# Performance work log

Hardware: AMD Instinct MI355X
Metric: run time of the kernel (lower is better)

The kernel has to match this reference:

```python
import jax, jax.numpy as jnp
import numpy as np

B, C, HH, WW, QK = 8, 64, 64, 64, 8


def setup_inputs() -> dict:
    key = jax.random.key(0)
    ks = jax.random.split(key, 22)
    s = 0.05
    def W(k, o, i):
        return jax.random.normal(k, (o, i), jnp.float32) * s
    def bvec(k, o):
        return jax.random.normal(k, (o,), jnp.float32) * s
    return {
        "H_in": jax.random.normal(ks[0], (B, C, HH, WW), jnp.float32),
        "M_prev": jax.random.normal(ks[1], (B, C, HH, WW), jnp.float32),
        "wq": W(ks[2], QK, C), "bq": bvec(ks[3], QK),
        "wkh": W(ks[4], QK, C), "bkh": bvec(ks[5], QK),
        "wvh": W(ks[6], C, C), "bvh": bvec(ks[7], C),
        "wkm": W(ks[8], QK, C), "bkm": bvec(ks[9], QK),
        "wvm": W(ks[10], C, C), "bvm": bvec(ks[11], C),
        "wz": W(ks[12], C, 2 * C), "bz": bvec(ks[13], C),
        "wo": W(ks[14], C, 2 * C), "bo": bvec(ks[15], C),
        "wg": W(ks[16], C, 2 * C), "bg": bvec(ks[17], C),
        "wi": W(ks[18], C, 2 * C), "bi": bvec(ks[19], C),
    }


def _conv1x1(w, b, x):
    # x: [B, Cin, N] -> [B, Cout, N]
    return jnp.einsum("oc,bcn->bon", w, x) + b[None, :, None]


def reference(H_in, M_prev, wq, bq, wkh, bkh, wvh, bvh, wkm, bkm, wvm, bvm,
              wz, bz, wo, bo, wg, bg, wi, bi):
    Bn, Cn, Hn, Wn = H_in.shape
    N = Hn * Wn
    h = H_in.reshape(Bn, Cn, N)   # flatten spatial
    m = M_prev.reshape(Bn, Cn, N)

    Q = _conv1x1(wq, bq, h)       # [B, QK, N]
    Kh = _conv1x1(wkh, bkh, h)
    Vh = _conv1x1(wvh, bvh, h)    # [B, C, N]
    Km = _conv1x1(wkm, bkm, m)
    Vm = _conv1x1(wvm, bvm, m)

    scale = jnp.asarray(np.sqrt(Q.shape[1]), Q.dtype)
    # scores: [B, N, N], softmax over last axis
    Ah = jax.nn.softmax(jnp.einsum("bcn,bcm->bnm", Q, Kh) / scale, axis=-1)
    Am = jax.nn.softmax(jnp.einsum("bcn,bcm->bnm", Q, Km) / scale, axis=-1)
    # Zh = Vh @ Ah^T : [B, C, N]
    Zh = jnp.einsum("bcm,bnm->bcn", Vh, Ah)
    Zm = jnp.einsum("bcm,bnm->bcn", Vm, Am)

    Z = _conv1x1(wz, bz, jnp.concatenate([Zh, Zm], axis=1))  # [B, C, N]
    concat = jnp.concatenate([h, Z], axis=1)                  # [B, 2C, N]
    O_t = jax.nn.sigmoid(_conv1x1(wo, bo, concat))
    G_t = jnp.tanh(_conv1x1(wg, bg, concat))
    I_t = jax.nn.sigmoid(_conv1x1(wi, bi, concat))

    M_t = (1.0 - I_t) * m + I_t * G_t
    H_out = O_t * M_t
    return (H_out.reshape(Bn, Cn, Hn, Wn), M_t.reshape(Bn, Cn, Hn, Wn))
```

## Files before the change

### kernel.cpp

```cpp
#include <hip/hip_runtime.h>

#define BATCH 8
#define CC 64
#define NN 4096
#define SCL 0.51006973f

typedef __attribute__((ext_vector_type(8))) short s16x8;
typedef __attribute__((ext_vector_type(4))) short s16x4;
typedef __attribute__((ext_vector_type(4))) float f32x4;
typedef __attribute__((ext_vector_type(2))) unsigned int uint2v;

__device__ __forceinline__ short f2bf(float f) {
  unsigned u = __builtin_bit_cast(unsigned, f);
  u += 0x7fffu + ((u >> 16) & 1u);
  return (short)(u >> 16);
}

__device__ __forceinline__ unsigned cvt_pk_bf16(float lo, float hi) {
  unsigned r;
  asm volatile("v_cvt_pk_bf16_f32 %0, %1, %2" : "=v"(r) : "v"(lo), "v"(hi));
  return r;
}

__device__ __forceinline__ int kperm(int kk) {
  int hh = (kk >> 5) & 1, g = (kk >> 3) & 3, c = kk & 7;
  return hh * 32 + (c < 4 ? (g << 2) + c : 16 + ((g ^ 2) << 2) + (c - 4));
}

__global__ void prep_weights_kernel(const float* __restrict__ wz, const float* __restrict__ bz,
                                    const float* __restrict__ wo, const float* __restrict__ bo,
                                    const float* __restrict__ wg, const float* __restrict__ bg,
                                    const float* __restrict__ wi, const float* __restrict__ bi,
                                    const float* __restrict__ wq, const float* __restrict__ bq,
                                    const float* __restrict__ wkh, const float* __restrict__ bkh,
                                    const float* __restrict__ wvh, const float* __restrict__ bvh,
                                    const float* __restrict__ wkm, const float* __restrict__ bkm,
                                    const float* __restrict__ wvm, const float* __restrict__ bvm,
                                    short* __restrict__ Weff, float* __restrict__ beff,
                                    short* __restrict__ Wcat, float* __restrict__ bias) {
  int i = blockIdx.x * 256 + threadIdx.x;
  const float* wjs[3] = {wo, wg, wi};
  const float* bjs[3] = {bo, bg, bi};
  const float gsc[3] = {1.44269504f, 2.88539008f, 1.44269504f};
  if (i < 36864) {
    int j = i / 12288, rem = i % 12288, o = rem / 192, k = rem % 192;
    const float* wj = wjs[j];
    float v;
    if (k < 64) {
      v = wj[o * 128 + k];
    } else {
      v = 0.f;
      #pragma unroll 8
      for (int t = 0; t < 64; ++t) v += wj[o * 128 + 64 + t] * wz[t * 128 + (k - 64)];
    }
    Weff[i] = f2bf(v * gsc[j]);
  } else if (i < 37056) {
    int i2 = i - 36864;
    int j = i2 >> 6, o = i2 & 63;
    const float* wj = wjs[j];
    float v = bjs[j][o];
    #pragma unroll 8
    for (int t = 0; t < 64; ++t) v += wj[o * 128 + 64 + t] * bz[t];
    beff[i2] = v * gsc[j];
  } else if (i < 47296) {
    int i2 = i - 37056;
    int src = i2 / 5120, rem = i2 % 5120, row = rem >> 6, col = rem & 63;
    float v;
    if (src == 0) {
      if (row < 64) v = wvh[row * 64 + col];
      else if (row < 72) v = wq[(row - 64) * 64 + col] * SCL;
      else v = wkh[(row - 72) * 64 + col];
    } else {
      if (row < 64) v = wvm[row * 64 + col];
      else if (row < 72) v = wkm[(row - 64) * 64 + col];
      else v = 0.f;
    }
    Wcat[i2] = f2bf(v);
  } else if (i < 47456) {
    int i3 = i - 47296;
    int src = i3 / 80, row = i3 % 80;
    float v;
    if (src == 0) v = (row < 64) ? bvh[row] : (row < 72 ? bq[row - 64] * SCL : bkh[row - 72]);
    else          v = (row < 64) ? bvm[row] : (row < 72 ? bkm[row - 64] : 0.f);
    bias[i3] = v;
  }
}

__global__ __launch_bounds__(256) void proj_kernel(
    const float* __restrict__ H_in, const float* __restrict__ M_prev,
    const short* __restrict__ Wcat, const float* __restrict__ bias,
    short* __restrict__ Qt, short* __restrict__ Kht, short* __restrict__ Kmt,
    short* __restrict__ Vh, short* __restrict__ Vm) {
  int src = blockIdx.x & 1;
  int n0 = ((blockIdx.x >> 1) & 31) << 7;
  int b = blockIdx.x >> 6;
  int tid = threadIdx.x, w = tid >> 6, l = tid & 63, lg = l >> 4, ll = l & 15;

  const float* __restrict__ X = src ? M_prev : H_in;
  short* __restrict__ Vp = src ? Vm : Vh;

  __shared__ __align__(16) short Xt[128][68];

  {
    int nl = tid & 127, chalf = (tid >> 7) << 5;
    int n = n0 + nl;
    #pragma unroll
    for (int cg = 0; cg < 8; ++cg) {
      int c = chalf + cg * 4;
      float v0 = X[((size_t)((b << 6) + c + 0)) * NN + n];
      float v1 = X[((size_t)((b << 6) + c + 1)) * NN + n];
      float v2 = X[((size_t)((b << 6) + c + 2)) * NN + n];
      float v3 = X[((size_t)((b << 6) + c + 3)) * NN + n];
      uint2v pk;
      pk.x = cvt_pk_bf16(v0, v1);
      pk.y = cvt_pk_bf16(v2, v3);
      *(uint2v*)&Xt[nl][c] = pk;
    }
  }
  __syncthreads();

  f32x4 acc[5][2];
  #pragma unroll
  for (int ot = 0; ot < 5; ++ot)
    #pragma unroll
    for (int ns = 0; ns < 2; ++ns)
      #pragma unroll
      for (int r = 0; r < 4; ++r) acc[ot][ns][r] = bias[src * 80 + ot * 16 + lg * 4 + r];

  #pragma unroll
  for (int kk = 0; kk < 2; ++kk) {
    s16x8 aw[5];
    #pragma unroll
    for (int ot = 0; ot < 5; ++ot)
      aw[ot] = *(const s16x8*)(Wcat + ((size_t)(src * 80 + ot * 16 + ll)) * 64 + kk * 32 + lg * 8);
    #pragma unroll
    for (int ns = 0; ns < 2; ++ns) {
      s16x8 bx = *(const s16x8*)&Xt[w * 32 + ns * 16 + ll][kk * 32 + lg * 8];
      #pragma unroll
      for (int ot = 0; ot < 5; ++ot)
        acc[ot][ns] = __builtin_amdgcn_mfma_f32_16x16x32_bf16(aw[ot], bx, acc[ot][ns], 0, 0, 0);
    }
  }

  #pragma unroll
  for (int ns = 0; ns < 2; ++ns) {
    int n = n0 + w * 32 + ns * 16 + ll;
    #pragma unroll
    for (int ot = 0; ot < 4; ++ot) {
      #pragma unroll
      for (int r = 0; r < 4; ++r) {
        int o = ot * 16 + lg * 4 + r;
        Vp[((size_t)((b << 6) + o)) * NN + n] = f2bf(acc[ot][ns][r]);
      }
    }
    int pr = (n & ~63) + kperm(n & 63);
    #pragma unroll
    for (int r = 0; r < 4; ++r) {
      float v = acc[4][ns][r];
      if (src == 0) {
        if (lg < 2) Qt[((size_t)(b * NN + n)) * 8 + (lg * 4 + r)] = f2bf(v);
        else        Kht[((size_t)(b * NN + pr)) * 8 + ((lg - 2) * 4 + r)] = f2bf(v);
      } else {
        if (lg < 2) Kmt[((size_t)(b * NN + pr)) * 8 + (lg * 4 + r)] = f2bf(v);
      }
    }
  }
}

__global__ __launch_bounds__(256) void attn_kernel(
    const short* __restrict__ Qt, const short* __restrict__ Kht, const short* __restrict__ Kmt,
    const short* __restrict__ Vh, const short* __restrict__ Vm, short* __restrict__ Zt) {
  unsigned vb = (blockIdx.x & 7) * 128 + (blockIdx.x >> 3);
  int b  = vb >> 7;
  int s  = (vb >> 6) & 1;
  int q0 = (vb & 63) << 6;
  int tid = threadIdx.x;
  int w = tid >> 6, l = tid & 63, lg = l >> 4, ll = l & 15;

  const short* __restrict__ Kp = s ? Kmt : Kht;
  const short* __restrict__ Vp = s ? Vm : Vh;

  __shared__ __align__(16) short Vt[2][64][128];
  __shared__ __align__(16) short Ktl[2][128][8];

  s16x8 bq = {};
  if (lg == 0) bq = *(const s16x8*)(Qt + ((size_t)(b * NN + q0 + w * 16 + ll)) * 8);
  s16x8 ones;
  #pragma unroll
  for (int i = 0; i < 8; ++i) ones[i] = (short)0x3F80;

  f32x4 accZ[4];
  f32x4 accDn = {0.f, 0.f, 0.f, 0.f};
  #pragma unroll
  for (int cs = 0; cs < 4; ++cs) accZ[cs] = (f32x4){0.f, 0.f, 0.f, 0.f};

  const bool lo32 = (l < 32);

  #define STAGE(buf_, k0_)                                                                   \
    do {                                                                                     \
      _Pragma("unroll")                                                                      \
      for (int j = 0; j < 4; ++j) {                                                          \
        int brow = j * 16 + w * 4;                                                           \
        int row = brow + (l >> 4);                                                           \
        int slot = l & 15;                                                                   \
        const short* src = Vp + ((size_t)((b << 6) + row)) * NN + (k0_) +                    \
                           ((slot ^ (row & 7)) << 3);                                        \
        __builtin_amdgcn_global_load_lds((const __attribute__((address_space(1))) void*)src, \
            (__attribute__((address_space(3))) void*)&Vt[buf_][brow][0], 16, 0, 0);          \
      }                                                                                      \
      if (w == 0) {                                                                          \
        _Pragma("unroll")                                                                    \
        for (int jk = 0; jk < 2; ++jk) {                                                     \
          const short* srck = Kp + ((size_t)(b * NN) + (k0_) + jk * 64 + l) * 8;             \
          __builtin_amdgcn_global_load_lds((const __attribute__((address_space(1))) void*)srck,\
              (__attribute__((address_space(3))) void*)&Ktl[buf_][jk * 64][0], 16, 0, 0);    \
        }                                                                                    \
      }                                                                                      \
    } while (0)

  STAGE(0, 0);
  int buf = 0;
  for (int kt = 0; kt < 32; ++kt) {
    asm volatile("s_waitcnt vmcnt(0)" ::: "memory");
    __builtin_amdgcn_s_barrier();
    if (kt < 31) { STAGE(buf ^ 1, (kt + 1) << 7); }

    #pragma unroll
    for (int s2 = 0; s2 < 2; ++s2) {
      float p[4][4];
      #pragma unroll
      for (int hh = 0; hh < 2; ++hh) {
        #pragma unroll
        for (int par = 0; par < 2; ++par) {
          s16x8 ak = *(const s16x8*)&Ktl[buf][s2 * 64 + hh * 32 + par * 16 + ll][0];
          f32x4 sc = __builtin_amdgcn_mfma_f32_16x16x32_bf16(ak, bq, (f32x4){0.f,0.f,0.f,0.f}, 0, 0, 0);
          #pragma unroll
          for (int r = 0; r < 4; ++r) p[hh * 2 + par][r] = __builtin_amdgcn_exp2f(sc[r]);
        }
      }
      unsigned wkv[4][2];
      #pragma unroll
      for (int ks = 0; ks < 4; ++ks) {
        wkv[ks][0] = cvt_pk_bf16(p[ks][0], p[ks][1]);
        wkv[ks][1] = cvt_pk_bf16(p[ks][2], p[ks][3]);
      }
      #pragma unroll
      for (int hh = 0; hh < 2; ++hh) {
        unsigned o0 = wkv[hh * 2 + 1][0], o1 = wkv[hh * 2 + 1][1];
        uint2v pr0 = __builtin_amdgcn_permlane32_swap(o0, o0, false, false);
        uint2v pr1 = __builtin_amdgcn_permlane32_swap(o1, o1, false, false);
        unsigned sw0 = lo32 ? pr0.y : pr0.x;
        unsigned sw1 = lo32 ? pr1.y : pr1.x;
        union { unsigned u[4]; s16x8 v; } bpu;
        bpu.u[0] = wkv[hh * 2][0];
        bpu.u[1] = wkv[hh * 2][1];
        bpu.u[2] = sw0;
        bpu.u[3] = sw1;
        s16x8 bp = bpu.v;
        accDn = __builtin_amdgcn_mfma_f32_16x16x32_bf16(ones, bp, accDn, 0, 0, 0);
        #pragma unroll
        for (int cs = 0; cs < 4; ++cs) {
          int row = cs * 16 + ll;
          int slot = (s2 << 3) + ((hh * 4 + lg) ^ (row & 7));
          s16x8 av = *(const s16x8*)((const short*)&Vt[buf][0][0] + row * 128 + slot * 8);
          accZ[cs] = __builtin_amdgcn_mfma_f32_16x16x32_bf16(av, bp, accZ[cs], 0, 0, 0);
        }
      }
    }
    buf ^= 1;
  }

  float rd = __builtin_amdgcn_rcpf(accDn[0]);
  #pragma unroll
  for (int cs = 0; cs < 4; ++cs) {
    s16x4 o4;
    #pragma unroll
    for (int r = 0; r < 4; ++r) o4[r] = f2bf(accZ[cs][r] * rd);
    *(s16x4*)(Zt + ((size_t)(b * NN + q0 + w * 16 + ll)) * 128 + s * 64 + cs * 16 + lg * 4) = o4;
  }
  #undef STAGE
}

__global__ __launch_bounds__(256) void gates_kernel(
    const float* __restrict__ H_in, const float* __restrict__ M_prev,
    const short* __restrict__ Zt, const short* __restrict__ Weff,
    const float* __restrict__ beff, float* __restrict__ out) {
  int b = blockIdx.x >> 6;
  int n0 = (blockIdx.x & 63) << 6;
  int tid = threadIdx.x, w = tid >> 6, l = tid & 63, lg = l >> 4, ll = l & 15;
  __shared__ __align__(16) short Xt[64][200];

  for (int i = tid; i < 512; i += 256) {
    int k = i >> 3, ns = i & 7;
    const float* src = H_in + ((size_t)((b << 6) + k)) * NN + n0 + ns * 8;
    #pragma unroll
    for (int j2 = 0; j2 < 8; ++j2) Xt[ns * 8 + j2][k] = f2bf(src[j2]);
  }
  for (int i = tid; i < 1024; i += 256) {
    int n = i >> 4, seg = i & 15;
    *(s16x8*)&Xt[n][64 + seg * 8] =
        *(const s16x8*)(Zt + ((size_t)(b * NN + n0 + n)) * 128 + seg * 8);
  }
  __syncthreads();

  f32x4 acc[3][4];
  #pragma unroll
  for (int j = 0; j < 3; ++j) {
    float bj = beff[j * 64 + w * 16 + lg * 4];
    float bj1 = beff[j * 64 + w * 16 + lg * 4 + 1];
    float bj2 = beff[j * 64 + w * 16 + lg * 4 + 2];
    float bj3 = beff[j * 64 + w * 16 + lg * 4 + 3];
    #pragma unroll
    for (int ns = 0; ns < 4; ++ns) {
      acc[j][ns][0] = bj; acc[j][ns][1] = bj1; acc[j][ns][2] = bj2; acc[j][ns][3] = bj3;
    }
  }

  #pragma unroll
  for (int kk = 0; kk < 6; ++kk) {
    s16x8 aw[3];
    #pragma unroll
    for (int j = 0; j < 3; ++j)
      aw[j] = *(const s16x8*)(Weff + ((size_t)(j * 64 + w * 16 + ll)) * 192 + kk * 32 + lg * 8);
    #pragma unroll
    for (int ns = 0; ns < 4; ++ns) {
      s16x8 bx = *(const s16x8*)&Xt[ns * 16 + ll][kk * 32 + lg * 8];
      #pragma unroll
      for (int j = 0; j < 3; ++j)
        acc[j][ns] = __builtin_amdgcn_mfma_f32_16x16x32_bf16(aw[j], bx, acc[j][ns], 0, 0, 0);
    }
  }

  float* Hout = out;
  float* Mout = out + (size_t)BATCH * CC * NN;
  #pragma unroll
  for (int ns = 0; ns < 4; ++ns) {
    #pragma unroll
    for (int r = 0; r < 4; ++r) {
      int c = w * 16 + lg * 4 + r;
      int n = n0 + ns * 16 + ll;
      size_t idx = ((size_t)((b << 6) + c)) * NN + n;
      float xo = acc[0][ns][r], xg = acc[1][ns][r], xi = acc[2][ns][r];
      float o  = __builtin_amdgcn_rcpf(1.f + __builtin_amdgcn_exp2f(-xo));
      float g  = 2.f * __builtin_amdgcn_rcpf(1.f + __builtin_amdgcn_exp2f(-xg)) - 1.f;
      float ii = __builtin_amdgcn_rcpf(1.f + __builtin_amdgcn_exp2f(-xi));
      float m  = M_prev[idx];
      float mt = (1.f - ii) * m + ii * g;
      Mout[idx] = mt;
      Hout[idx] = o * mt;
    }
  }
}

extern "C" void kernel_launch(void* const* d_in, const int* in_sizes, int n_in,
                              void* d_out, int out_size, void* d_ws, size_t ws_size,
                              hipStream_t stream) {
  (void)in_sizes; (void)n_in; (void)out_size; (void)ws_size;
  const float* H_in  = (const float*)d_in[0];
  const float* M_prev= (const float*)d_in[1];
  const float* wq  = (const float*)d_in[2];
  const float* bq  = (const float*)d_in[3];
  const float* wkh = (const float*)d_in[4];
  const float* bkh = (const float*)d_in[5];
  const float* wvh = (const float*)d_in[6];
  const float* bvh = (const float*)d_in[7];
  const float* wkm = (const float*)d_in[8];
  const float* bkm = (const float*)d_in[9];
  const float* wvm = (const float*)d_in[10];
  const float* bvm = (const float*)d_in[11];
  const float* wz  = (const float*)d_in[12];
  const float* bz  = (const float*)d_in[13];
  const float* wo  = (const float*)d_in[14];
  const float* bo  = (const float*)d_in[15];
  const float* wg  = (const float*)d_in[16];
  const float* bg  = (const float*)d_in[17];
  const float* wi  = (const float*)d_in[18];
  const float* bi  = (const float*)d_in[19];

  char* ws = (char*)d_ws;
  size_t off = 0;
  auto alloc = [&](size_t bytes) -> void* {
    void* p = ws + off;
    off += (bytes + 255) & ~(size_t)255;
    return p;
  };
  short* Weff = (short*)alloc(3 * 64 * 192 * 2);
  float* beff = (float*)alloc(192 * 4);
  short* Wcat = (short*)alloc(2 * 80 * 64 * 2);
  float* bias = (float*)alloc(160 * 4);
  short* Qt   = (short*)alloc((size_t)BATCH * NN * 8 * 2);
  short* Kht  = (short*)alloc((size_t)BATCH * NN * 8 * 2);
  short* Kmt  = (short*)alloc((size_t)BATCH * NN * 8 * 2);
  short* Vh   = (short*)alloc((size_t)BATCH * CC * NN * 2);
  short* Vm   = (short*)alloc((size_t)BATCH * CC * NN * 2);
  short* Zt   = (short*)alloc((size_t)BATCH * NN * 128 * 2);

  prep_weights_kernel<<<186, 256, 0, stream>>>(wz, bz, wo, bo, wg, bg, wi, bi,
                                               wq, bq, wkh, bkh, wvh, bvh, wkm, bkm, wvm, bvm,
                                               Weff, beff, Wcat, bias);
  proj_kernel<<<512, 256, 0, stream>>>(H_in, M_prev, Wcat, bias, Qt, Kht, Kmt, Vh, Vm);
  attn_kernel<<<1024, 256, 0, stream>>>(Qt, Kht, Kmt, Vh, Vm, Zt);
  gates_kernel<<<512, 256, 0, stream>>>(H_in, M_prev, Zt, Weff, beff, (float*)d_out);
}
```

Before: 190.3 us.

## Split attention key range across two blocks and combine partials in gates kernel

The attention kernel now splits the 4096 keys into two halves handled by separate blocks, doubling the grid to 2048 blocks. Each block writes unnormalized partial Z and denominators, and the gates kernel sums the two halves and normalizes. Shared-memory tiles shrink to 64 keys and launch bounds request 6 blocks per SU for higher occupancy. The projection kernel also writes a bf16 transposed copy of H so the gates kernel avoids the strided fp32 transpose, and gates uses smaller 32-column tiles. The cost is extra global traffic for the partial Z buffers and denominators.

Result: no change. 189.7 us (-0.3%).

```diff
diff --git a/kernel.cpp b/kernel.cpp
--- a/kernel.cpp
+++ b/kernel.cpp
@@ -15,7 +15,10 @@
   u += 0x7fffu + ((u >> 16) & 1u);
   return (short)(u >> 16);
 }
-
+__device__ __forceinline__ float bf2f(short h) {
+  unsigned u = ((unsigned)(unsigned short)h) << 16;
+  return __builtin_bit_cast(float, u);
+}
 __device__ __forceinline__ unsigned cvt_pk_bf16(float lo, float hi) {
   unsigned r;
   asm volatile("v_cvt_pk_bf16_f32 %0, %1, %2" : "=v"(r) : "v"(lo), "v"(hi));
@@ -90,7 +93,7 @@
     const float* __restrict__ H_in, const float* __restrict__ M_prev,
     const short* __restrict__ Wcat, const float* __restrict__ bias,
     short* __restrict__ Qt, short* __restrict__ Kht, short* __restrict__ Kmt,
-    short* __restrict__ Vh, short* __restrict__ Vm) {
+    short* __restrict__ Vh, short* __restrict__ Vm, short* __restrict__ Ht) {
   int src = blockIdx.x & 1;
   int n0 = ((blockIdx.x >> 1) & 31) << 7;
   int b = blockIdx.x >> 6;
@@ -119,6 +122,15 @@
   }
   __syncthreads();
 
+  if (src == 0) {
+    #pragma unroll
+    for (int j = 0; j < 4; ++j) {
+      int ci = tid + j * 256;
+      int n = ci >> 3, seg = ci & 7;
+      *(s16x8*)(Ht + ((size_t)(b * NN + n0 + n)) * 64 + seg * 8) = *(const s16x8*)&Xt[n][seg * 8];
+    }
+  }
+
   f32x4 acc[5][2];
   #pragma unroll
   for (int ot = 0; ot < 5; ++ot)
@@ -167,21 +179,26 @@
   }
 }
 
-__global__ __launch_bounds__(256) void attn_kernel(
+__global__ __launch_bounds__(256, 6) void attn_kernel(
     const short* __restrict__ Qt, const short* __restrict__ Kht, const short* __restrict__ Kmt,
-    const short* __restrict__ Vh, const short* __restrict__ Vm, short* __restrict__ Zt) {
-  unsigned vb = (blockIdx.x & 7) * 128 + (blockIdx.x >> 3);
-  int b  = vb >> 7;
+    const short* __restrict__ Vh, const short* __restrict__ Vm,
+    short* __restrict__ Zp, float* __restrict__ dnb) {
+  unsigned vb = (blockIdx.x & 7) * 256 + (blockIdx.x >> 3);
+  int kh = vb >> 10;
+  int b  = (vb >> 7) & 7;
   int s  = (vb >> 6) & 1;
   int q0 = (vb & 63) << 6;
   int tid = threadIdx.x;
   int w = tid >> 6, l = tid & 63, lg = l >> 4, ll = l & 15;
+  const bool lo32 = (l < 32);
 
   const short* __restrict__ Kp = s ? Kmt : Kht;
   const short* __restrict__ Vp = s ? Vm : Vh;
 
-  __shared__ __align__(16) short Vt[2][64][128];
-  __shared__ __align__(16) short Ktl[2][128][8];
+  __shared__ __align__(16) short Vt[2][64][64];
+  __shared__ __align__(16) short Ktl[2][64][8];
+  short* VtF = &Vt[0][0][0];
+  short* KtF = &Ktl[0][0][0];
 
   s16x8 bq = {};
   if (lg == 0) bq = *(const s16x8*)(Qt + ((size_t)(b * NN + q0 + w * 16 + ll)) * 8);
@@ -194,127 +211,136 @@
   #pragma unroll
   for (int cs = 0; cs < 4; ++cs) accZ[cs] = (f32x4){0.f, 0.f, 0.f, 0.f};
 
-  const bool lo32 = (l < 32);
-
-  #define STAGE(buf_, k0_)                                                                   \
-    do {                                                                                     \
-      _Pragma("unroll")                                                                      \
-      for (int j = 0; j < 4; ++j) {                                                          \
-        int brow = j * 16 + w * 4;                                                           \
-        int row = brow + (l >> 4);                                                           \
-        int slot = l & 15;                                                                   \
-        const short* src = Vp + ((size_t)((b << 6) + row)) * NN + (k0_) +                    \
-                           ((slot ^ (row & 7)) << 3);                                        \
-        __builtin_amdgcn_global_load_lds((const __attribute__((address_space(1))) void*)src, \
-            (__attribute__((address_space(3))) void*)&Vt[buf_][brow][0], 16, 0, 0);          \
-      }                                                                                      \
-      if (w == 0) {                                                                          \
-        _Pragma("unroll")                                                                    \
-        for (int jk = 0; jk < 2; ++jk) {                                                     \
-          const short* srck = Kp + ((size_t)(b * NN) + (k0_) + jk * 64 + l) * 8;             \
-          __builtin_amdgcn_global_load_lds((const __attribute__((address_space(1))) void*)srck,\
-              (__attribute__((address_space(3))) void*)&Ktl[buf_][jk * 64][0], 16, 0, 0);    \
-        }                                                                                    \
-      }                                                                                      \
-    } while (0)
+  const int vOff0 = ll * 64 + ((lg ^ (ll & 7)) << 3);
+  const int vOff1 = ll * 64 + (((lg ^ 4) ^ (ll & 7)) << 3);
+  const int kOff  = ll * 8;
+
+  const int row0 = w * 8 + (l >> 3);
+  const int swz  = ((l & 7) ^ (l >> 3)) << 3;
+  const short* vsrc0 = Vp + ((size_t)((b << 6) + row0)) * NN + kh * 2048 + swz;
+  const short* vsrc1 = Vp + ((size_t)((b << 6) + 32 + row0)) * NN + kh * 2048 + swz;
+  const short* ksrc  = Kp + ((size_t)(b * NN) + kh * 2048 + l) * 8;
+
+#define GLDS(src_, dst_) \
+  __builtin_amdgcn_global_load_lds((const __attribute__((address_space(1))) void*)(src_), \
+                                   (__attribute__((address_space(3))) void*)(dst_), 16, 0, 0)
+#define STAGE(bufL, ktL) do { \
+    GLDS(vsrc0 + (ktL) * 64, VtF + (bufL) * 4096 + w * 512); \
+    GLDS(vsrc1 + (ktL) * 64, VtF + (bufL) * 4096 + 2048 + w * 512); \
+    if (w == 0) GLDS(ksrc + (ktL) * 512, KtF + (bufL) * 512); \
+  } while (0)
+
+  auto compute = [&](int bufL) {
+    float p[4][4];
+    #pragma unroll
+    for (int hh = 0; hh < 2; ++hh) {
+      #pragma unroll
+      for (int par = 0; par < 2; ++par) {
+        s16x8 ak = *(const s16x8*)(KtF + bufL * 512 + (hh * 32 + par * 16) * 8 + kOff);
+        f32x4 sc = __builtin_amdgcn_mfma_f32_16x16x32_bf16(ak, bq, (f32x4){0.f,0.f,0.f,0.f}, 0, 0, 0);
+        #pragma unroll
+        for (int r = 0; r < 4; ++r) p[hh * 2 + par][r] = __builtin_amdgcn_exp2f(sc[r]);
+      }
+    }
+    unsigned wkv[4][2];
+    #pragma unroll
+    for (int ks = 0; ks < 4; ++ks) {
+      wkv[ks][0] = cvt_pk_bf16(p[ks][0], p[ks][1]);
+      wkv[ks][1] = cvt_pk_bf16(p[ks][2], p[ks][3]);
+    }
+    #pragma unroll
+    for (int hh = 0; hh < 2; ++hh) {
+      unsigned o0 = wkv[hh * 2 + 1][0], o1 = wkv[hh * 2 + 1][1];
+      uint2v pr0 = __builtin_amdgcn_permlane32_swap(o0, o0, false, false);
+      uint2v pr1 = __builtin_amdgcn_permlane32_swap(o1, o1, false, false);
+      unsigned sw0 = lo32 ? pr0.y : pr0.x;
+      unsigned sw1 = lo32 ? pr1.y : pr1.x;
+      union { unsigned u[4]; s16x8 v; } bpu;
+      bpu.u[0] = wkv[hh * 2][0];
+      bpu.u[1] = wkv[hh * 2][1];
+      bpu.u[2] = sw0;
+      bpu.u[3] = sw1;
+      s16x8 bp = bpu.v;
+      accDn = __builtin_amdgcn_mfma_f32_16x16x32_bf16(ones, bp, accDn, 0, 0, 0);
+      const int vo = hh ? vOff1 : vOff0;
+      #pragma unroll
+      for (int cs = 0; cs < 4; ++cs) {
+        s16x8 av = *(const s16x8*)(VtF + bufL * 4096 + cs * 1024 + vo);
+        accZ[cs] = __builtin_amdgcn_mfma_f32_16x16x32_bf16(av, bp, accZ[cs], 0, 0, 0);
+      }
+    }
+  };
 
   STAGE(0, 0);
-  int buf = 0;
-  for (int kt = 0; kt < 32; ++kt) {
+  #pragma unroll 1
+  for (int kt2 = 0; kt2 < 16; ++kt2) {
+    int kt = kt2 * 2;
     asm volatile("s_waitcnt vmcnt(0)" ::: "memory");
     __builtin_amdgcn_s_barrier();
-    if (kt < 31) { STAGE(buf ^ 1, (kt + 1) << 7); }
-
-    #pragma unroll
-    for (int s2 = 0; s2 < 2; ++s2) {
-      float p[4][4];
-      #pragma unroll
-      for (int hh = 0; hh < 2; ++hh) {
-        #pragma unroll
-        for (int par = 0; par < 2; ++par) {
-          s16x8 ak = *(const s16x8*)&Ktl[buf][s2 * 64 + hh * 32 + par * 16 + ll][0];
-          f32x4 sc = __builtin_amdgcn_mfma_f32_16x16x32_bf16(ak, bq, (f32x4){0.f,0.f,0.f,0.f}, 0, 0, 0);
-          #pragma unroll
-          for (int r = 0; r < 4; ++r) p[hh * 2 + par][r] = __builtin_amdgcn_exp2f(sc[r]);
-        }
-      }
-      unsigned wkv[4][2];
-      #pragma unroll
-      for (int ks = 0; ks < 4; ++ks) {
-        wkv[ks][0] = cvt_pk_bf16(p[ks][0], p[ks][1]);
-        wkv[ks][1] = cvt_pk_bf16(p[ks][2], p[ks][3]);
-      }
-      #pragma unroll
-      for (int hh = 0; hh < 2; ++hh) {
-        unsigned o0 = wkv[hh * 2 + 1][0], o1 = wkv[hh * 2 + 1][1];
-        uint2v pr0 = __builtin_amdgcn_permlane32_swap(o0, o0, false, false);
-        uint2v pr1 = __builtin_amdgcn_permlane32_swap(o1, o1, false, false);
-        unsigned sw0 = lo32 ? pr0.y : pr0.x;
-        unsigned sw1 = lo32 ? pr1.y : pr1.x;
-        union { unsigned u[4]; s16x8 v; } bpu;
-        bpu.u[0] = wkv[hh * 2][0];
-        bpu.u[1] = wkv[hh * 2][1];
-        bpu.u[2] = sw0;
-        bpu.u[3] = sw1;
-        s16x8 bp = bpu.v;
-        accDn = __builtin_amdgcn_mfma_f32_16x16x32_bf16(ones, bp, accDn, 0, 0, 0);
-        #pragma unroll
-        for (int cs = 0; cs < 4; ++cs) {
-          int row = cs * 16 + ll;
-          int slot = (s2 << 3) + ((hh * 4 + lg) ^ (row & 7));
-          s16x8 av = *(const s16x8*)((const short*)&Vt[buf][0][0] + row * 128 + slot * 8);
-          accZ[cs] = __builtin_amdgcn_mfma_f32_16x16x32_bf16(av, bp, accZ[cs], 0, 0, 0);
-        }
-      }
-    }
-    buf ^= 1;
-  }
-
-  float rd = __builtin_amdgcn_rcpf(accDn[0]);
+    STAGE(1, kt + 1);
+    compute(0);
+    asm volatile("s_waitcnt vmcnt(0)" ::: "memory");
+    __builtin_amdgcn_s_barrier();
+    if (kt2 < 15) STAGE(0, kt + 2);
+    compute(1);
+  }
+
   #pragma unroll
   for (int cs = 0; cs < 4; ++cs) {
     s16x4 o4;
     #pragma unroll
-    for (int r = 0; r < 4; ++r) o4[r] = f2bf(accZ[cs][r] * rd);
-    *(s16x4*)(Zt + ((size_t)(b * NN + q0 + w * 16 + ll)) * 128 + s * 64 + cs * 16 + lg * 4) = o4;
-  }
-  #undef STAGE
+    for (int r = 0; r < 4; ++r) o4[r] = f2bf(accZ[cs][r]);
+    *(s16x4*)(Zp + ((size_t)((kh * 8 + b) * NN + q0 + w * 16 + ll)) * 128 + s * 64 + cs * 16 + lg * 4) = o4;
+  }
+  if (l < 16)
+    dnb[((size_t)(kh * 16 + b * 2 + s)) * NN + q0 + w * 16 + l] = accDn[0];
+#undef STAGE
+#undef GLDS
 }
 
 __global__ __launch_bounds__(256) void gates_kernel(
-    const float* __restrict__ H_in, const float* __restrict__ M_prev,
-    const short* __restrict__ Zt, const short* __restrict__ Weff,
-    const float* __restrict__ beff, float* __restrict__ out) {
-  int b = blockIdx.x >> 6;
-  int n0 = (blockIdx.x & 63) << 6;
+    const float* __restrict__ M_prev, const short* __restrict__ Ht,
+    const short* __restrict__ Zp, const float* __restrict__ dnb,
+    const short* __restrict__ Weff, const float* __restrict__ beff,
+    float* __restrict__ out) {
+  int b = blockIdx.x >> 7;
+  int n0 = (blockIdx.x & 127) << 5;
   int tid = threadIdx.x, w = tid >> 6, l = tid & 63, lg = l >> 4, ll = l & 15;
-  __shared__ __align__(16) short Xt[64][200];
-
-  for (int i = tid; i < 512; i += 256) {
-    int k = i >> 3, ns = i & 7;
-    const float* src = H_in + ((size_t)((b << 6) + k)) * NN + n0 + ns * 8;
-    #pragma unroll
-    for (int j2 = 0; j2 < 8; ++j2) Xt[ns * 8 + j2][k] = f2bf(src[j2]);
-  }
-  for (int i = tid; i < 1024; i += 256) {
-    int n = i >> 4, seg = i & 15;
-    *(s16x8*)&Xt[n][64 + seg * 8] =
-        *(const s16x8*)(Zt + ((size_t)(b * NN + n0 + n)) * 128 + seg * 8);
+  __shared__ __align__(16) short Xt[32][200];
+
+  {
+    int n = tid >> 3, seg = tid & 7;
+    *(s16x8*)&Xt[n][seg * 8] = *(const s16x8*)(Ht + ((size_t)(b * NN + n0 + n)) * 64 + seg * 8);
+  }
+  {
+    int n = tid >> 3, cq = tid & 7, sidx = cq >> 2;
+    const short* z0 = Zp + ((size_t)(b * NN + n0 + n)) * 128 + cq * 16;
+    const short* z1 = Zp + ((size_t)((8 + b) * NN + n0 + n)) * 128 + cq * 16;
+    float d0 = dnb[((size_t)(b * 2 + sidx)) * NN + n0 + n];
+    float d1 = dnb[((size_t)(16 + b * 2 + sidx)) * NN + n0 + n];
+    float rd = __builtin_amdgcn_rcpf(d0 + d1);
+    s16x8 a0 = *(const s16x8*)z0;
+    s16x8 a1 = *(const s16x8*)z1;
+    s16x8 b0 = *(const s16x8*)(z0 + 8);
+    s16x8 b1 = *(const s16x8*)(z1 + 8);
+    s16x8 o0, o1;
+    #pragma unroll
+    for (int j = 0; j < 8; ++j) {
+      o0[j] = f2bf((bf2f(a0[j]) + bf2f(a1[j])) * rd);
+      o1[j] = f2bf((bf2f(b0[j]) + bf2f(b1[j])) * rd);
+    }
+    *(s16x8*)&Xt[n][64 + cq * 16] = o0;
+    *(s16x8*)&Xt[n][64 + cq * 16 + 8] = o1;
   }
   __syncthreads();
 
-  f32x4 acc[3][4];
-  #pragma unroll
-  for (int j = 0; j < 3; ++j) {
-    float bj = beff[j * 64 + w * 16 + lg * 4];
-    float bj1 = beff[j * 64 + w * 16 + lg * 4 + 1];
-    float bj2 = beff[j * 64 + w * 16 + lg * 4 + 2];
-    float bj3 = beff[j * 64 + w * 16 + lg * 4 + 3];
-    #pragma unroll
-    for (int ns = 0; ns < 4; ++ns) {
-      acc[j][ns][0] = bj; acc[j][ns][1] = bj1; acc[j][ns][2] = bj2; acc[j][ns][3] = bj3;
-    }
-  }
+  f32x4 acc[3][2];
+  #pragma unroll
+  for (int j = 0; j < 3; ++j)
+    #pragma unroll
+    for (int ns = 0; ns < 2; ++ns)
+      #pragma unroll
+      for (int r = 0; r < 4; ++r) acc[j][ns][r] = beff[j * 64 + w * 16 + lg * 4 + r];
 
   #pragma unroll
   for (int kk = 0; kk < 6; ++kk) {
@@ -323,7 +349,7 @@
     for (int j = 0; j < 3; ++j)
       aw[j] = *(const s16x8*)(Weff + ((size_t)(j * 64 + w * 16 + ll)) * 192 + kk * 32 + lg * 8);
     #pragma unroll
-    for (int ns = 0; ns < 4; ++ns) {
+    for (int ns = 0; ns < 2; ++ns) {
       s16x8 bx = *(const s16x8*)&Xt[ns * 16 + ll][kk * 32 + lg * 8];
       #pragma unroll
       for (int j = 0; j < 3; ++j)
@@ -334,7 +360,7 @@
   float* Hout = out;
   float* Mout = out + (size_t)BATCH * CC * NN;
   #pragma unroll
-  for (int ns = 0; ns < 4; ++ns) {
+  for (int ns = 0; ns < 2; ++ns) {
     #pragma unroll
     for (int r = 0; r < 4; ++r) {
       int c = w * 16 + lg * 4 + r;
@@ -393,12 +419,14 @@
   short* Kmt  = (short*)alloc((size_t)BATCH * NN * 8 * 2);
   short* Vh   = (short*)alloc((size_t)BATCH * CC * NN * 2);
   short* Vm   = (short*)alloc((size_t)BATCH * CC * NN * 2);
-  short* Zt   = (short*)alloc((size_t)BATCH * NN * 128 * 2);
+  short* Ht   = (short*)alloc((size_t)BATCH * NN * 64 * 2);
+  short* Zp   = (short*)alloc((size_t)2 * BATCH * NN * 128 * 2);
+  float* dnb  = (float*)alloc((size_t)2 * BATCH * 2 * NN * 4);
 
   prep_weights_kernel<<<186, 256, 0, stream>>>(wz, bz, wo, bo, wg, bg, wi, bi,
                                                wq, bq, wkh, bkh, wvh, bvh, wkm, bkm, wvm, bvm,
                                                Weff, beff, Wcat, bias);
-  proj_kernel<<<512, 256, 0, stream>>>(H_in, M_prev, Wcat, bias, Qt, Kht, Kmt, Vh, Vm);
-  attn_kernel<<<1024, 256, 0, stream>>>(Qt, Kht, Kmt, Vh, Vm, Zt);
-  gates_kernel<<<512, 256, 0, stream>>>(H_in, M_prev, Zt, Weff, beff, (float*)d_out);
-}
+  proj_kernel<<<512, 256, 0, stream>>>(H_in, M_prev, Wcat, bias, Qt, Kht, Kmt, Vh, Vm, Ht);
+  attn_kernel<<<2048, 256, 0, stream>>>(Qt, Kht, Kmt, Vh, Vm, Zp, dnb);
+  gates_kernel<<<1024, 256, 0, stream>>>(M_prev, Ht, Zp, dnb, Weff, beff, (float*)d_out);
+}
```
